# Performance work log

Hardware: AMD Instinct MI355X
Metric: run time of the kernel (lower is better)

Reference implementation:

```python
import jax, jax.numpy as jnp
import numpy as np

V, E, H, C, M, CLS = 32000, 300, 512, 256, 512, 1
B, T = 64, 128
NEG = -1e9


def setup_inputs() -> dict:
    key = jax.random.key(0)
    ks = jax.random.split(key, 16)
    u = lambda k, shape, r: jax.random.uniform(k, shape, jnp.float32, -r, r)
    klstm = 1.0 / np.sqrt(H)
    inp = {
        "s1": jax.random.randint(ks[0], (B, T), 0, V, dtype=jnp.int32),
        "s2": jax.random.randint(ks[1], (B, T), 0, V, dtype=jnp.int32),
        "s1_length": jax.random.randint(ks[2], (B,), 1, T + 1, dtype=jnp.int32),
        "s2_length": jax.random.randint(ks[3], (B,), 1, T + 1, dtype=jnp.int32),
        "s1_h0": jnp.zeros((2, B, H), jnp.float32),
        "s1_c0": jnp.zeros((2, B, H), jnp.float32),
        "s2_h0": jnp.zeros((2, B, H), jnp.float32),
        "s2_c0": jnp.zeros((2, B, H), jnp.float32),
        "emb": jax.random.normal(ks[4], (V, E), jnp.float32) * 0.1,
        "Wih_f": u(ks[5], (4 * H, E), klstm),
        "Whh_f": u(ks[6], (4 * H, H), klstm),
        "b_f": u(ks[7], (4 * H,), klstm),
        "Wih_b": u(ks[8], (4 * H, E), klstm),
        "Whh_b": u(ks[9], (4 * H, H), klstm),
        "b_b": u(ks[10], (4 * H,), klstm),
        "S1W": u(ks[11], (C, 2 * H), 0.1),
        "S2W": u(ks[12], (1, C), 0.1),
        "mlpW": u(ks[13], (M, 4 * H), 0.1),
        "mlpb": jnp.zeros((M,), jnp.float32),
        "outW": u(ks[14], (CLS, M), 0.1),
        "outb": jnp.zeros((CLS,), jnp.float32),
    }
    return inp


def lstm(x, h0, c0, Wih, Whh, b):
    # x: [B,T,E] -> outputs [B,T,H]; PyTorch gate order i,f,g,o
    xW = jnp.einsum("bte,ge->btg", x, Wih) + b  # [B,T,4H]

    def step(carry, xw):
        h, c = carry
        g = xw + h @ Whh.T
        i, f, gg, o = jnp.split(g, 4, axis=-1)
        c = jax.nn.sigmoid(f) * c + jax.nn.sigmoid(i) * jnp.tanh(gg)
        h = jax.nn.sigmoid(o) * jnp.tanh(c)
        return (h, c), h

    _, hs = jax.lax.scan(step, (h0, c0), jnp.swapaxes(xW, 0, 1))
    return jnp.swapaxes(hs, 0, 1)


def encode(tokens, lens, h0, c0, emb, Wih_f, Whh_f, b_f, Wih_b, Whh_b, b_b, S1W, S2W):
    x = emb[tokens]  # [B,T,E]
    t = jnp.arange(tokens.shape[1])
    # reverse-within-valid-length indices (pack/pad semantics for bwd direction)
    idx = jnp.where(t[None, :] < lens[:, None], lens[:, None] - 1 - t[None, :], t[None, :])
    out_f = lstm(x, h0[0], c0[0], Wih_f, Whh_f, b_f)
    x_rev = jnp.take_along_axis(x, idx[:, :, None], axis=1)
    out_b = lstm(x_rev, h0[1], c0[1], Wih_b, Whh_b, b_b)
    out_b = jnp.take_along_axis(out_b, idx[:, :, None], axis=1)
    Hout = jnp.concatenate([out_f, out_b], axis=-1)  # [B,T,2H]
    # attention pooling: S2(tanh(S1(H))), softmax over valid positions
    scores = jnp.einsum("btc,c->bt", jnp.tanh(jnp.einsum("btd,cd->btc", Hout, S1W)), S2W[0])
    scores = jnp.where(t[None, :] < lens[:, None], scores, NEG)
    attn = jax.nn.softmax(scores, axis=1)
    return jnp.einsum("bt,btd->bd", attn, Hout)  # [B,2H]


def reference(s1, s2, s1_length, s2_length, s1_h0, s1_c0, s2_h0, s2_c0, emb,
              Wih_f, Whh_f, b_f, Wih_b, Whh_b, b_b, S1W, S2W, mlpW, mlpb, outW, outb):
    r1 = encode(s1, s1_length, s1_h0, s1_c0, emb, Wih_f, Whh_f, b_f, Wih_b, Whh_b, b_b, S1W, S2W)
    r2 = encode(s2, s2_length, s2_h0, s2_c0, emb, Wih_f, Whh_f, b_f, Wih_b, Whh_b, b_b, S1W, S2W)
    merged = jnp.concatenate([r1 + r2, (r1 - r2) ** 2], axis=1)  # [B,4H]
    out_mlp = merged @ mlpW.T + mlpb  # no activation, per original
    return jax.nn.sigmoid(out_mlp @ outW.T + outb)  # [B,CLS]
```

## Files before the change

### kernel.cpp

```cpp
#include <hip/hip_runtime.h>
#include <hip/hip_bf16.h>

#define B_  64
#define T_  128
#define E_  300
#define EP  320
#define H_  512
#define G4  2048
#define R_  128
#define C_  256
#define M_  512
#define TS  (T_ + 1)
#define NB  128
#define SENT 0xFFFFFFFFFFFFFFFFULL

typedef short bf16x8 __attribute__((ext_vector_type(8)));
typedef float f32x4  __attribute__((ext_vector_type(4)));
#define MFMA(a, b, c) __builtin_amdgcn_mfma_f32_16x16x32_bf16((a), (b), (c), 0, 0, 0)

__device__ __forceinline__ float fsig(float x) { return 1.0f / (1.0f + __expf(-x)); }
__device__ __forceinline__ float ftanh(float x) {
    float a = fminf(fabsf(x), 15.0f);
    float e = __expf(2.0f * a);
    return copysignf((e - 1.0f) / (e + 1.0f), x);
}
__device__ __forceinline__ ushort f2bf(float f) {
    __hip_bfloat16 h = __float2bfloat16(f);
    return *reinterpret_cast<ushort*>(&h);
}
__device__ __forceinline__ float bf2f(ushort u) {
    __hip_bfloat16 h = *reinterpret_cast<__hip_bfloat16*>(&u);
    return __bfloat162float(h);
}

__global__ __launch_bounds__(256) void k_cvt_all(
    const float* __restrict__ emb,
    const float* __restrict__ Wih_f, const float* __restrict__ Wih_b,
    const float* __restrict__ Whh_f, const float* __restrict__ Whh_b,
    const float* __restrict__ S1W,
    const float* __restrict__ s1_h0, const float* __restrict__ s2_h0,
    ushort* __restrict__ embB,
    ushort* __restrict__ WihBf, ushort* __restrict__ WihBb,
    ushort* __restrict__ WhhBf, ushort* __restrict__ WhhBb,
    ushort* __restrict__ S1WB,
    ushort* __restrict__ hfB, ushort* __restrict__ hbB)
{
    const int b = blockIdx.x;
    if (b >= 5056) {
        const int r = b - 5056;
        const int rl = (r < B_) ? r : r - B_;
        const float* h0 = (r < B_) ? s1_h0 : s2_h0;
        for (int u = threadIdx.x; u < 128; u += 256) {
            const int which = u >> 6;
            const int c8 = (u & 63) * 8;
            const float* s = h0 + (long)which * B_ * H_ + (long)rl * H_ + c8;
            ushort* d = (which ? hbB : hfB) + (long)r * TS * H_ + c8;
            float4 f0 = *(const float4*)&s[0];
            float4 f1 = *(const float4*)&s[4];
            bf16x8 v;
            v[0] = (short)f2bf(f0.x); v[1] = (short)f2bf(f0.y);
            v[2] = (short)f2bf(f0.z); v[3] = (short)f2bf(f0.w);
            v[4] = (short)f2bf(f1.x); v[5] = (short)f2bf(f1.y);
            v[6] = (short)f2bf(f1.z); v[7] = (short)f2bf(f1.w);
            *(bf16x8*)d = v;
        }
        return;
    }
    const float* src; ushort* dst; int r0, sk, dk;
    if (b < 4000)      { src = emb;   dst = embB;  r0 = b * 8;          sk = E_;    dk = EP; }
    else if (b < 4256) { src = Wih_f; dst = WihBf; r0 = (b - 4000) * 8; sk = E_;    dk = EP; }
    else if (b < 4512) { src = Wih_b; dst = WihBb; r0 = (b - 4256) * 8; sk = E_;    dk = EP; }
    else if (b < 4768) { src = Whh_f; dst = WhhBf; r0 = (b - 4512) * 8; sk = H_;    dk = H_; }
    else if (b < 5024) { src = Whh_b; dst = WhhBb; r0 = (b - 4768) * 8; sk = H_;    dk = H_; }
    else               { src = S1W;   dst = S1WB;  r0 = (b - 5024) * 8; sk = 2*H_;  dk = 2*H_; }
    const int upr = dk >> 3;
    for (int u = threadIdx.x; u < 8 * upr; u += 256) {
        const int r  = r0 + u / upr;
        const int c8 = (u % upr) * 8;
        const float* s = &src[(long)r * sk + c8];
        bf16x8 v;
        if (c8 + 8 <= sk) {
            float4 f0 = *(const float4*)&s[0];
            float4 f1 = *(const float4*)&s[4];
            v[0] = (short)f2bf(f0.x); v[1] = (short)f2bf(f0.y);
            v[2] = (short)f2bf(f0.z); v[3] = (short)f2bf(f0.w);
            v[4] = (short)f2bf(f1.x); v[5] = (short)f2bf(f1.y);
            v[6] = (short)f2bf(f1.z); v[7] = (short)f2bf(f1.w);
        } else {
#pragma unroll
            for (int e = 0; e < 8; ++e)
                v[e] = (c8 + e < sk) ? (short)f2bf(s[e]) : (short)0;
        }
        *(bf16x8*)&dst[(long)r * dk + c8] = v;
    }
}

__global__ __launch_bounds__(256) void k_embed_mfma(
    const int* __restrict__ s1, const int* __restrict__ s2,
    const int* __restrict__ l1, const int* __restrict__ l2,
    const ushort* __restrict__ embB,
    const ushort* __restrict__ WihBf, const ushort* __restrict__ WihBb,
    const float* __restrict__ b_f, const float* __restrict__ b_b,
    ushort* __restrict__ xf, ushort* __restrict__ xb)
{
    const int dir = blockIdx.z;
    const int r   = blockIdx.y >> 1;
    const int t0  = (blockIdx.y & 1) * 64;
    const int N0  = blockIdx.x * 256;
    const int L   = (r < B_) ? l1[r] : l2[r - B_];
    if (L <= t0) return;

    const int tid = threadIdx.x;
    const int lane = tid & 63, w = tid >> 6;
    const int wm = w & 1, wn = w >> 1;
    const int l15 = lane & 15, q8 = (lane >> 4) * 8;

    __shared__ int toks[64];
    __shared__ __align__(16) ushort As[64][72];
    __shared__ __align__(16) ushort Bs[256][72];

    if (tid < 64) {
        int t  = t0 + tid;
        int tt = dir ? ((t < L) ? (L - 1 - t) : t) : t;
        toks[tid] = (r < B_) ? s1[r * T_ + tt] : s2[(r - B_) * T_ + tt];
    }
    __syncthreads();

    const ushort* Wih  = dir ? WihBb : WihBf;
    const float*  bias = dir ? b_b : b_f;

    f32x4 acc[2][8] = {};

    for (int k0 = 0; k0 < EP; k0 += 64) {
#pragma unroll
        for (int p = 0; p < 2; ++p) {
            int u = tid + p * 256;
            int row = u >> 3, seg = u & 7;
            *(uint4*)&As[row][seg * 8] =
                *(const uint4*)&embB[(long)toks[row] * EP + k0 + seg * 8];
        }
#pragma unroll
        for (int p = 0; p < 8; ++p) {
            int u = tid + p * 256;
            int row = u >> 3, seg = u & 7;
            *(uint4*)&Bs[row][seg * 8] =
                *(const uint4*)&Wih[(long)(N0 + row) * EP + k0 + seg * 8];
        }
        __syncthreads();
#pragma unroll
        for (int ks = 0; ks < 2; ++ks) {
            bf16x8 af[2], bfr[8];
#pragma unroll
            for (int mt = 0; mt < 2; ++mt)
                af[mt] = *(const bf16x8*)&As[wm * 32 + mt * 16 + l15][ks * 32 + q8];
#pragma unroll
            for (int nt = 0; nt < 8; ++nt)
                bfr[nt] = *(const bf16x8*)&Bs[wn * 128 + nt * 16 + l15][ks * 32 + q8];
#pragma unroll
            for (int mt = 0; mt < 2; ++mt)
#pragma unroll
                for (int nt = 0; nt < 8; ++nt)
                    acc[mt][nt] = MFMA(af[mt], bfr[nt], acc[mt][nt]);
        }
        __syncthreads();
    }

    ushort* xout = dir ? xb : xf;
#pragma unroll
    for (int mt = 0; mt < 2; ++mt) {
        int m = r * T_ + t0 + wm * 32 + mt * 16 + (lane >> 4) * 4;
#pragma unroll
        for (int nt = 0; nt < 8; ++nt) {
            int col = N0 + wn * 128 + nt * 16 + l15;
            float bv = bias[col];
#pragma unroll
            for (int rg = 0; rg < 4; ++rg) {
                uint v = f2bf(acc[mt][nt][rg] + bv);
                uint pv = (uint)__shfl_xor((int)v, 1);
                if (!(lane & 1))
                    *(uint*)&xout[(long)(m + rg) * G4 + col] = v | (pv << 16);
            }
        }
    }
}

__global__ __launch_bounds__(256) void k_recur(
    const ushort* __restrict__ xf, const ushort* __restrict__ xb,
    ushort* __restrict__ hfB, ushort* __restrict__ hbB,
    const ushort* __restrict__ WhhBf, const ushort* __restrict__ WhhBb,
    const float* __restrict__ s1_c0, const float* __restrict__ s2_c0)
{
    const int bx = blockIdx.x;
    const int s  = bx >> 6;
    const int rb = (bx >> 4) & 3;
    const int jb = bx & 15;
    const int r0 = rb * 32, j0 = jb * 32;

    const ushort* xW  = s ? xb : xf;
    const ushort* Whh = s ? WhhBb : WhhBf;
    ushort* hB = s ? hbB : hfB;

    const int tid = threadIdx.x;
    const int lane = tid & 63;
    const int g = tid >> 6;
    const int l15 = lane & 15, q8 = (lane >> 4) * 8;

    __shared__ __align__(16) ushort As[32][520];
    __shared__ float Gs[4][32][33];

    bf16x8 bfr[2][16];
#pragma unroll
    for (int nt = 0; nt < 2; ++nt) {
        const ushort* brow = &Whh[((long)g * H_ + j0 + nt * 16 + l15) * H_];
#pragma unroll
        for (int ks = 0; ks < 16; ++ks)
            bfr[nt][ks] = *(const bf16x8*)&brow[ks * 32 + q8];
    }

    const int rr = tid >> 3, jj = (tid & 7) * 4;
    const int rg_ = r0 + rr;
    const int rl  = (rg_ < B_) ? rg_ : rg_ - B_;
    const float* c0p = (rg_ < B_) ? s1_c0 : s2_c0;
    float cst[4];
#pragma unroll
    for (int cc = 0; cc < 4; ++cc)
        cst[cc] = c0p[(long)s * B_ * H_ + (long)rl * H_ + j0 + jj + cc];

    const int arow = tid >> 3, aseg = tid & 7;
    const int swz = ((aseg + arow) & 7) * 8;

    for (int t = 0; t < T_; ++t) {
        uint2 xw[4];
        const long xbase = ((long)rg_ * T_ + t) * G4 + j0 + jj;
#pragma unroll
        for (int gg = 0; gg < 4; ++gg)
            xw[gg] = *(const uint2*)&xW[xbase + gg * H_];

        const ushort* hrow = &hB[((long)(r0 + arow) * TS + t) * H_ + aseg * 8];
        unsigned long long hv[16];
        bool ok;
        do {
#pragma unroll
            for (int i = 0; i < 16; ++i) {
                const unsigned long long* p8 =
                    (const unsigned long long*)(hrow + (i >> 1) * 64 + (i & 1) * 4);
                hv[i] = __hip_atomic_load(p8, __ATOMIC_RELAXED,
                                          __HIP_MEMORY_SCOPE_AGENT);
            }
            ok = true;
#pragma unroll
            for (int i = 0; i < 16; ++i)
                ok = ok && (hv[i] != SENT);
        } while (!ok);

#pragma unroll
        for (int sl = 0; sl < 8; ++sl) {
            uint4 av;
            av.x = (uint)hv[2 * sl];       av.y = (uint)(hv[2 * sl] >> 32);
            av.z = (uint)hv[2 * sl + 1];   av.w = (uint)(hv[2 * sl + 1] >> 32);
            *(uint4*)&As[arow][sl * 64 + swz] = av;
        }
        __syncthreads();

        f32x4 acc[2][2] = {};
#pragma unroll
        for (int ks = 0; ks < 16; ++ks) {
            const int e  = ks * 32 + q8;
            const int sl = e >> 6;
            const int c  = (e >> 3) & 7;
            bf16x8 a0 = *(const bf16x8*)&As[l15][sl * 64 + (((c + l15) & 7) << 3)];
            bf16x8 a1 = *(const bf16x8*)&As[16 + l15][sl * 64 + (((c + l15) & 7) << 3)];
            acc[0][0] = MFMA(a0, bfr[0][ks], acc[0][0]);
            acc[0][1] = MFMA(a0, bfr[1][ks], acc[0][1]);
            acc[1][0] = MFMA(a1, bfr[0][ks], acc[1][0]);
            acc[1][1] = MFMA(a1, bfr[1][ks], acc[1][1]);
        }

#pragma unroll
        for (int mt = 0; mt < 2; ++mt)
#pragma unroll
            for (int nt = 0; nt < 2; ++nt)
#pragma unroll
                for (int rg2 = 0; rg2 < 4; ++rg2)
                    Gs[g][mt * 16 + (lane >> 4) * 4 + rg2][nt * 16 + l15] =
                        acc[mt][nt][rg2];
        __syncthreads();

        ushort hp[4];
#pragma unroll
        for (int cc = 0; cc < 4; ++cc) {
            uint xv0 = (cc < 2) ? xw[0].x : xw[0].y;
            uint xv1 = (cc < 2) ? xw[1].x : xw[1].y;
            uint xv2 = (cc < 2) ? xw[2].x : xw[2].y;
            uint xv3 = (cc < 2) ? xw[3].x : xw[3].y;
            int sh = (cc & 1) * 16;
            float gi = Gs[0][rr][jj + cc] + bf2f((ushort)(xv0 >> sh));
            float gf = Gs[1][rr][jj + cc] + bf2f((ushort)(xv1 >> sh));
            float gg = Gs[2][rr][jj + cc] + bf2f((ushort)(xv2 >> sh));
            float go = Gs[3][rr][jj + cc] + bf2f((ushort)(xv3 >> sh));
            cst[cc] = fsig(gf) * cst[cc] + fsig(gi) * ftanh(gg);
            hp[cc] = f2bf(fsig(go) * ftanh(cst[cc]));
        }
        unsigned long long pk = (unsigned long long)hp[0]
                              | ((unsigned long long)hp[1] << 16)
                              | ((unsigned long long)hp[2] << 32)
                              | ((unsigned long long)hp[3] << 48);
        __hip_atomic_store(
            (unsigned long long*)&hB[((long)rg_ * TS + t + 1) * H_ + j0 + jj],
            pk, __ATOMIC_RELAXED, __HIP_MEMORY_SCOPE_AGENT);
    }
}

__global__ __launch_bounds__(256) void k_attn_fused(
    const ushort* __restrict__ hfB, const ushort* __restrict__ hbB,
    const int* __restrict__ l1, const int* __restrict__ l2,
    const ushort* __restrict__ S1WB, const float* __restrict__ S2W,
    float* __restrict__ pooled)
{
    const int r = blockIdx.x;
    const int L = (r < B_) ? l1[r] : l2[r - B_];
    const int tid = threadIdx.x;
    const int lane = tid & 63, w = tid >> 6;
    const int wm = w & 1, wn = w >> 1;
    const int l15 = lane & 15, q8 = (lane >> 4) * 8;

    __shared__ __align__(16) ushort As[128][72];
    __shared__ __align__(16) ushort Bs[256][72];
    __shared__ float sc[T_];
    __shared__ float att[T_];

    if (tid < T_) sc[tid] = 0.0f;

    f32x4 acc[4][8] = {};

    for (int k0 = 0; k0 < 2 * H_; k0 += 64) {
#pragma unroll
        for (int p = 0; p < 4; ++p) {
            int u = tid + p * 256;
            int row = u >> 3, seg = u & 7;
            int k = k0 + seg * 8;
            long idx;
            const ushort* src;
            if (k0 < H_) {
                src = hfB; idx = ((long)r * TS + row + 1) * H_ + k;
            } else {
                int tt = (row < L) ? (L - 1 - row) : row;
                src = hbB; idx = ((long)r * TS + tt + 1) * H_ + (k - H_);
            }
            *(uint4*)&As[row][seg * 8] = *(const uint4*)&src[idx];
        }
#pragma unroll
        for (int p = 0; p < 8; ++p) {
            int u = tid + p * 256;
            int row = u >> 3, seg = u & 7;
            *(uint4*)&Bs[row][seg * 8] =
                *(const uint4*)&S1WB[(long)row * (2 * H_) + k0 + seg * 8];
        }
        __syncthreads();
#pragma unroll
        for (int ks = 0; ks < 2; ++ks) {
            bf16x8 af[4], bfr[8];
#pragma unroll
            for (int mt = 0; mt < 4; ++mt)
                af[mt] = *(const bf16x8*)&As[wm * 64 + mt * 16 + l15][ks * 32 + q8];
#pragma unroll
            for (int nt = 0; nt < 8; ++nt)
                bfr[nt] = *(const bf16x8*)&Bs[wn * 128 + nt * 16 + l15][ks * 32 + q8];
#pragma unroll
            for (int mt = 0; mt < 4; ++mt)
#pragma unroll
                for (int nt = 0; nt < 8; ++nt)
                    acc[mt][nt] = MFMA(af[mt], bfr[nt], acc[mt][nt]);
        }
        __syncthreads();
    }

    float s2r[8];
#pragma unroll
    for (int nt = 0; nt < 8; ++nt)
        s2r[nt] = S2W[wn * 128 + nt * 16 + l15];
#pragma unroll
    for (int mt = 0; mt < 4; ++mt)
#pragma unroll
        for (int rg = 0; rg < 4; ++rg) {
            float v = 0.0f;
#pragma unroll
            for (int nt = 0; nt < 8; ++nt)
                v += ftanh(acc[mt][nt][rg]) * s2r[nt];
            v += __shfl_xor(v, 1);
            v += __shfl_xor(v, 2);
            v += __shfl_xor(v, 4);
            v += __shfl_xor(v, 8);
            if (l15 == 0)
                atomicAdd(&sc[wm * 64 + mt * 16 + (lane >> 4) * 4 + rg], v);
        }
    __syncthreads();

    float mx = -1e30f;
    for (int tt = 0; tt < L; ++tt) mx = fmaxf(mx, sc[tt]);
    __syncthreads();
    if (tid < T_) att[tid] = (tid < L) ? __expf(sc[tid] - mx) : 0.0f;
    __syncthreads();
    float sum = 0.0f;
    for (int tt = 0; tt < L; ++tt) sum += att[tt];
    float inv = 1.0f / sum;

    for (int p = tid; p < 512; p += 256) {
        float a0 = 0.0f, a1 = 0.0f;
        if (p < 256) {
            int d = p * 2;
            for (int tt = 0; tt < L; ++tt) {
                uint hv = *(const uint*)&hfB[((long)r * TS + tt + 1) * H_ + d];
                a0 += att[tt] * bf2f((ushort)(hv & 0xffff));
                a1 += att[tt] * bf2f((ushort)(hv >> 16));
            }
            pooled[(long)r * (2 * H_) + d]     = a0 * inv;
            pooled[(long)r * (2 * H_) + d + 1] = a1 * inv;
        } else {
            int d = (p - 256) * 2;
            for (int tt = 0; tt < L; ++tt) {
                uint hv = *(const uint*)&hbB[((long)r * TS + (L - tt)) * H_ + d];
                a0 += att[tt] * bf2f((ushort)(hv & 0xffff));
                a1 += att[tt] * bf2f((ushort)(hv >> 16));
            }
            pooled[(long)r * (2 * H_) + H_ + d]     = a0 * inv;
            pooled[(long)r * (2 * H_) + H_ + d + 1] = a1 * inv;
        }
    }
}

__global__ __launch_bounds__(256) void k_mlp1(
    const float* __restrict__ pooled,
    const float* __restrict__ mlpW, const float* __restrict__ mlpb,
    float* __restrict__ om)
{
    const int mg = blockIdx.x;
    const int b  = blockIdx.y;
    const int tid = threadIdx.x;
    const int lane = tid & 63, w = tid >> 6;

    __shared__ __align__(16) float sm[2048];

#pragma unroll
    for (int it = 0; it < 8; ++it) {
        int d = tid + it * 256;
        float v;
        if (d < 1024) {
            v = pooled[(long)b * 1024 + d] + pooled[(long)(B_ + b) * 1024 + d];
        } else {
            int dd = d - 1024;
            float x = pooled[(long)b * 1024 + dd] - pooled[(long)(B_ + b) * 1024 + dd];
            v = x * x;
        }
        sm[d] = v;
    }
    __syncthreads();

    for (int i = 0; i < 16; ++i) {
        int mm = mg * 64 + w * 16 + i;
        const float* wrow = &mlpW[(long)mm * 2048];
        float ax = 0.f, ay = 0.f, az = 0.f, aw = 0.f;
#pragma unroll
        for (int it = 0; it < 8; ++it) {
            int k = it * 256 + lane * 4;
            float4 wv = *(const float4*)&wrow[k];
            float4 sv = *(const float4*)&sm[k];
            ax += wv.x * sv.x; ay += wv.y * sv.y;
            az += wv.z * sv.z; aw += wv.w * sv.w;
        }
        float ssum = (ax + ay) + (az + aw);
        for (int off = 32; off; off >>= 1) ssum += __shfl_down(ssum, off);
        if (lane == 0) om[(long)b * M_ + mm] = ssum + mlpb[mm];
    }
}

__global__ __launch_bounds__(256) void k_final(
    const float* __restrict__ om,
    const float* __restrict__ outW, const float* __restrict__ outb,
    float* __restrict__ out)
{
    const int b = blockIdx.x;
    const int tid = threadIdx.x;
    __shared__ float red[256];
    float p = om[(long)b * M_ + tid] * outW[tid]
            + om[(long)b * M_ + 256 + tid] * outW[256 + tid];
    red[tid] = p;
    __syncthreads();
    for (int off = 128; off > 0; off >>= 1) {
        if (tid < off) red[tid] += red[tid + off];
        __syncthreads();
    }
    if (tid == 0) out[b] = 1.0f / (1.0f + __expf(-(red[0] + outb[0])));
}

extern "C" void kernel_launch(void* const* d_in, const int* in_sizes, int n_in,
                              void* d_out, int out_size, void* d_ws, size_t ws_size,
                              hipStream_t stream)
{
    const int*   s1    = (const int*)d_in[0];
    const int*   s2    = (const int*)d_in[1];
    const int*   l1    = (const int*)d_in[2];
    const int*   l2    = (const int*)d_in[3];
    const float* s1_h0 = (const float*)d_in[4];
    const float* s1_c0 = (const float*)d_in[5];
    const float* s2_h0 = (const float*)d_in[6];
    const float* s2_c0 = (const float*)d_in[7];
    const float* emb   = (const float*)d_in[8];
    const float* Wih_f = (const float*)d_in[9];
    const float* Whh_f = (const float*)d_in[10];
    const float* b_f   = (const float*)d_in[11];
    const float* Wih_b = (const float*)d_in[12];
    const float* Whh_b = (const float*)d_in[13];
    const float* b_b   = (const float*)d_in[14];
    const float* S1W   = (const float*)d_in[15];
    const float* S2W   = (const float*)d_in[16];
    const float* mlpW  = (const float*)d_in[17];
    const float* mlpb  = (const float*)d_in[18];
    const float* outW  = (const float*)d_in[19];
    const float* outb  = (const float*)d_in[20];
    float* out = (float*)d_out;

    ushort* p16 = (ushort*)d_ws;
    ushort* embB  = p16;  p16 += (long)32000 * EP;
    ushort* WihBf = p16;  p16 += (long)G4 * EP;
    ushort* WihBb = p16;  p16 += (long)G4 * EP;
    ushort* WhhBf = p16;  p16 += (long)G4 * H_;
    ushort* WhhBb = p16;  p16 += (long)G4 * H_;
    ushort* S1WB  = p16;  p16 += (long)C_ * 2 * H_;
    ushort* xf    = p16;  p16 += (long)R_ * T_ * G4;
    ushort* xb    = p16;  p16 += (long)R_ * T_ * G4;
    ushort* hfB   = p16;  p16 += (long)R_ * TS * H_;
    ushort* hbB   = p16;  p16 += (long)R_ * TS * H_;
    float* pf = (float*)p16;
    float* pooled = pf;   pf += (long)R_ * 2 * H_;
    float* om     = pf;   pf += (long)B_ * M_;

    hipMemsetAsync(hfB, 0xFF, (size_t)2 * R_ * TS * H_ * sizeof(ushort), stream);

    k_cvt_all<<<5184, 256, 0, stream>>>(emb, Wih_f, Wih_b, Whh_f, Whh_b, S1W,
                                        s1_h0, s2_h0,
                                        embB, WihBf, WihBb, WhhBf, WhhBb, S1WB,
                                        hfB, hbB);

    k_embed_mfma<<<dim3(8, 256, 2), 256, 0, stream>>>(
        s1, s2, l1, l2, embB, WihBf, WihBb, b_f, b_b, xf, xb);

    k_recur<<<NB, 256, 0, stream>>>(xf, xb, hfB, hbB, WhhBf, WhhBb,
                                    s1_c0, s2_c0);

    k_attn_fused<<<R_, 256, 0, stream>>>(hfB, hbB, l1, l2, S1WB, S2W, pooled);

    k_mlp1<<<dim3(8, B_), 256, 0, stream>>>(pooled, mlpW, mlpb, om);
    k_final<<<B_, 256, 0, stream>>>(om, outW, outb, out);
}
```

Baseline: 791.6 us.

## Fuse input projection into recurrent kernel, computing next step's xW during recurrence

Drops the separate embedding-projection GEMM kernel and its large xf/xb intermediate buffers. Each recurrent block now keeps its slice of Wih in LDS, gathers the next timestep's embeddings, and computes the input projection for step t+1 with MFMA while waiting inside the serial recurrence. This removes the global round trip for the precomputed gates and one kernel launch. In exchange it adds per-step work and LDS traffic to the latency-critical recurrent loop, and it raises LDS use (about 100KB per block).

```diff
diff --git a/kernel.cpp b/kernel.cpp
--- a/kernel.cpp
+++ b/kernel.cpp
@@ -95,97 +95,12 @@
     }
 }
 
-__global__ __launch_bounds__(256) void k_embed_mfma(
+__global__ __launch_bounds__(256, 1) void k_recur(
     const int* __restrict__ s1, const int* __restrict__ s2,
     const int* __restrict__ l1, const int* __restrict__ l2,
     const ushort* __restrict__ embB,
     const ushort* __restrict__ WihBf, const ushort* __restrict__ WihBb,
     const float* __restrict__ b_f, const float* __restrict__ b_b,
-    ushort* __restrict__ xf, ushort* __restrict__ xb)
-{
-    const int dir = blockIdx.z;
-    const int r   = blockIdx.y >> 1;
-    const int t0  = (blockIdx.y & 1) * 64;
-    const int N0  = blockIdx.x * 256;
-    const int L   = (r < B_) ? l1[r] : l2[r - B_];
-    if (L <= t0) return;
-
-    const int tid = threadIdx.x;
-    const int lane = tid & 63, w = tid >> 6;
-    const int wm = w & 1, wn = w >> 1;
-    const int l15 = lane & 15, q8 = (lane >> 4) * 8;
-
-    __shared__ int toks[64];
-    __shared__ __align__(16) ushort As[64][72];
-    __shared__ __align__(16) ushort Bs[256][72];
-
-    if (tid < 64) {
-        int t  = t0 + tid;
-        int tt = dir ? ((t < L) ? (L - 1 - t) : t) : t;
-        toks[tid] = (r < B_) ? s1[r * T_ + tt] : s2[(r - B_) * T_ + tt];
-    }
-    __syncthreads();
-
-    const ushort* Wih  = dir ? WihBb : WihBf;
-    const float*  bias = dir ? b_b : b_f;
-
-    f32x4 acc[2][8] = {};
-
-    for (int k0 = 0; k0 < EP; k0 += 64) {
-#pragma unroll
-        for (int p = 0; p < 2; ++p) {
-            int u = tid + p * 256;
-            int row = u >> 3, seg = u & 7;
-            *(uint4*)&As[row][seg * 8] =
-                *(const uint4*)&embB[(long)toks[row] * EP + k0 + seg * 8];
-        }
-#pragma unroll
-        for (int p = 0; p < 8; ++p) {
-            int u = tid + p * 256;
-            int row = u >> 3, seg = u & 7;
-            *(uint4*)&Bs[row][seg * 8] =
-                *(const uint4*)&Wih[(long)(N0 + row) * EP + k0 + seg * 8];
-        }
-        __syncthreads();
-#pragma unroll
-        for (int ks = 0; ks < 2; ++ks) {
-            bf16x8 af[2], bfr[8];
-#pragma unroll
-            for (int mt = 0; mt < 2; ++mt)
-                af[mt] = *(const bf16x8*)&As[wm * 32 + mt * 16 + l15][ks * 32 + q8];
-#pragma unroll
-            for (int nt = 0; nt < 8; ++nt)
-                bfr[nt] = *(const bf16x8*)&Bs[wn * 128 + nt * 16 + l15][ks * 32 + q8];
-#pragma unroll
-            for (int mt = 0; mt < 2; ++mt)
-#pragma unroll
-                for (int nt = 0; nt < 8; ++nt)
-                    acc[mt][nt] = MFMA(af[mt], bfr[nt], acc[mt][nt]);
-        }
-        __syncthreads();
-    }
-
-    ushort* xout = dir ? xb : xf;
-#pragma unroll
-    for (int mt = 0; mt < 2; ++mt) {
-        int m = r * T_ + t0 + wm * 32 + mt * 16 + (lane >> 4) * 4;
-#pragma unroll
-        for (int nt = 0; nt < 8; ++nt) {
-            int col = N0 + wn * 128 + nt * 16 + l15;
-            float bv = bias[col];
-#pragma unroll
-            for (int rg = 0; rg < 4; ++rg) {
-                uint v = f2bf(acc[mt][nt][rg] + bv);
-                uint pv = (uint)__shfl_xor((int)v, 1);
-                if (!(lane & 1))
-                    *(uint*)&xout[(long)(m + rg) * G4 + col] = v | (pv << 16);
-            }
-        }
-    }
-}
-
-__global__ __launch_bounds__(256) void k_recur(
-    const ushort* __restrict__ xf, const ushort* __restrict__ xb,
     ushort* __restrict__ hfB, ushort* __restrict__ hbB,
     const ushort* __restrict__ WhhBf, const ushort* __restrict__ WhhBb,
     const float* __restrict__ s1_c0, const float* __restrict__ s2_c0)
@@ -196,8 +111,9 @@
     const int jb = bx & 15;
     const int r0 = rb * 32, j0 = jb * 32;
 
-    const ushort* xW  = s ? xb : xf;
-    const ushort* Whh = s ? WhhBb : WhhBf;
+    const ushort* Whh  = s ? WhhBb : WhhBf;
+    const ushort* WihB = s ? WihBb : WihBf;
+    const float*  bias = s ? b_b : b_f;
     ushort* hB = s ? hbB : hfB;
 
     const int tid = threadIdx.x;
@@ -207,6 +123,11 @@
 
     __shared__ __align__(16) ushort As[32][520];
     __shared__ float Gs[4][32][33];
+    __shared__ __align__(16) ushort WihL[128 * 320];
+    __shared__ __align__(16) ushort Aemb[32 * 320];
+    __shared__ __align__(16) ushort xWs[4][32][36];
+    __shared__ int toks[32];
+    __shared__ int Ls[32];
 
     bf16x8 bfr[2][16];
 #pragma unroll
@@ -229,12 +150,66 @@
     const int arow = tid >> 3, aseg = tid & 7;
     const int swz = ((aseg + arow) & 7) * 8;
 
+    const float biasv0 = bias[g * H_ + j0 + l15];
+    const float biasv1 = bias[g * H_ + j0 + 16 + l15];
+    const int cr0 = g * 32 + l15, cr1 = g * 32 + 16 + l15;
+
+    if (tid < 32) {
+        int rg = r0 + tid;
+        int L = (rg < B_) ? l1[rg] : l2[rg - B_];
+        Ls[tid] = L;
+        int tt = s ? ((L > 0) ? L - 1 : 0) : 0;
+        toks[tid] = (rg < B_) ? s1[rg * T_ + tt] : s2[(rg - B_) * T_ + tt];
+    }
+    for (int u = tid; u < 5120; u += 256) {
+        int cr = u / 40, un = u % 40;
+        int grow = (cr >> 5) * H_ + j0 + (cr & 31);
+        int pos = (un >> 3) * 64 + ((((un & 7) + cr) & 7) << 3);
+        *(bf16x8*)&WihL[cr * 320 + pos] =
+            *(const bf16x8*)&WihB[(long)grow * EP + un * 8];
+    }
+    __syncthreads();
+    for (int u = tid; u < 1280; u += 256) {
+        int row = u / 40, un = u % 40;
+        int pos = (un >> 3) * 64 + ((((un & 7) + row) & 7) << 3);
+        *(bf16x8*)&Aemb[row * 320 + pos] =
+            *(const bf16x8*)&embB[(long)toks[row] * EP + un * 8];
+    }
+    __syncthreads();
+    {
+        f32x4 ax[2][2] = {};
+#pragma unroll
+        for (int kk = 0; kk < 10; ++kk) {
+            int e = kk * 32 + q8;
+            int sb = (e >> 6) * 64;
+            int ch = (e >> 3) & 7;
+            bf16x8 a0 = *(const bf16x8*)&Aemb[l15 * 320 + sb + (((ch + l15) & 7) << 3)];
+            bf16x8 a1 = *(const bf16x8*)&Aemb[(16 + l15) * 320 + sb + (((ch + 16 + l15) & 7) << 3)];
+            bf16x8 b0 = *(const bf16x8*)&WihL[cr0 * 320 + sb + (((ch + cr0) & 7) << 3)];
+            bf16x8 b1 = *(const bf16x8*)&WihL[cr1 * 320 + sb + (((ch + cr1) & 7) << 3)];
+            ax[0][0] = MFMA(a0, b0, ax[0][0]);
+            ax[0][1] = MFMA(a0, b1, ax[0][1]);
+            ax[1][0] = MFMA(a1, b0, ax[1][0]);
+            ax[1][1] = MFMA(a1, b1, ax[1][1]);
+        }
+#pragma unroll
+        for (int mt = 0; mt < 2; ++mt)
+#pragma unroll
+            for (int rgx = 0; rgx < 4; ++rgx) {
+                int row = mt * 16 + (lane >> 4) * 4 + rgx;
+                xWs[g][row][l15]      = f2bf(ax[mt][0][rgx] + biasv0);
+                xWs[g][row][16 + l15] = f2bf(ax[mt][1][rgx] + biasv1);
+            }
+    }
+    __syncthreads();
+
     for (int t = 0; t < T_; ++t) {
-        uint2 xw[4];
-        const long xbase = ((long)rg_ * T_ + t) * G4 + j0 + jj;
-#pragma unroll
-        for (int gg = 0; gg < 4; ++gg)
-            xw[gg] = *(const uint2*)&xW[xbase + gg * H_];
+        if (t + 1 < T_ && tid < 32) {
+            int L = Ls[tid], tq = t + 1;
+            int tt = s ? ((tq < L) ? L - 1 - tq : tq) : tq;
+            int rg = r0 + tid;
+            toks[tid] = (rg < B_) ? s1[rg * T_ + tt] : s2[(rg - B_) * T_ + tt];
+        }
 
         const ushort* hrow = &hB[((long)(r0 + arow) * TS + t) * H_ + aseg * 8];
         unsigned long long hv[16];
@@ -261,6 +236,11 @@
             *(uint4*)&As[arow][sl * 64 + swz] = av;
         }
         __syncthreads();
+
+        uint2 xwr[4];
+#pragma unroll
+        for (int gg = 0; gg < 4; ++gg)
+            xwr[gg] = *(const uint2*)&xWs[gg][rr][jj];
 
         f32x4 acc[2][2] = {};
 #pragma unroll
@@ -276,6 +256,15 @@
             acc[1][1] = MFMA(a1, bfr[1][ks], acc[1][1]);
         }
 
+        if (t + 1 < T_) {
+            for (int u = tid; u < 1280; u += 256) {
+                int row = u / 40, un = u % 40;
+                int pos = (un >> 3) * 64 + ((((un & 7) + row) & 7) << 3);
+                *(bf16x8*)&Aemb[row * 320 + pos] =
+                    *(const bf16x8*)&embB[(long)toks[row] * EP + un * 8];
+            }
+        }
+
 #pragma unroll
         for (int mt = 0; mt < 2; ++mt)
 #pragma unroll
@@ -286,13 +275,39 @@
                         acc[mt][nt][rg2];
         __syncthreads();
 
+        if (t + 1 < T_) {
+            f32x4 ax[2][2] = {};
+#pragma unroll
+            for (int kk = 0; kk < 10; ++kk) {
+                int e = kk * 32 + q8;
+                int sb = (e >> 6) * 64;
+                int ch = (e >> 3) & 7;
+                bf16x8 a0 = *(const bf16x8*)&Aemb[l15 * 320 + sb + (((ch + l15) & 7) << 3)];
+                bf16x8 a1 = *(const bf16x8*)&Aemb[(16 + l15) * 320 + sb + (((ch + 16 + l15) & 7) << 3)];
+                bf16x8 b0 = *(const bf16x8*)&WihL[cr0 * 320 + sb + (((ch + cr0) & 7) << 3)];
+                bf16x8 b1 = *(const bf16x8*)&WihL[cr1 * 320 + sb + (((ch + cr1) & 7) << 3)];
+                ax[0][0] = MFMA(a0, b0, ax[0][0]);
+                ax[0][1] = MFMA(a0, b1, ax[0][1]);
+                ax[1][0] = MFMA(a1, b0, ax[1][0]);
+                ax[1][1] = MFMA(a1, b1, ax[1][1]);
+            }
+#pragma unroll
+            for (int mt = 0; mt < 2; ++mt)
+#pragma unroll
+                for (int rgx = 0; rgx < 4; ++rgx) {
+                    int row = mt * 16 + (lane >> 4) * 4 + rgx;
+                    xWs[g][row][l15]      = f2bf(ax[mt][0][rgx] + biasv0);
+                    xWs[g][row][16 + l15] = f2bf(ax[mt][1][rgx] + biasv1);
+                }
+        }
+
         ushort hp[4];
 #pragma unroll
         for (int cc = 0; cc < 4; ++cc) {
-            uint xv0 = (cc < 2) ? xw[0].x : xw[0].y;
-            uint xv1 = (cc < 2) ? xw[1].x : xw[1].y;
-            uint xv2 = (cc < 2) ? xw[2].x : xw[2].y;
-            uint xv3 = (cc < 2) ? xw[3].x : xw[3].y;
+            uint xv0 = (cc < 2) ? xwr[0].x : xwr[0].y;
+            uint xv1 = (cc < 2) ? xwr[1].x : xwr[1].y;
+            uint xv2 = (cc < 2) ? xwr[2].x : xwr[2].y;
+            uint xv3 = (cc < 2) ? xwr[3].x : xwr[3].y;
             int sh = (cc & 1) * 16;
             float gi = Gs[0][rr][jj + cc] + bf2f((ushort)(xv0 >> sh));
             float gf = Gs[1][rr][jj + cc] + bf2f((ushort)(xv1 >> sh));
@@ -527,8 +542,6 @@
     ushort* WhhBf = p16;  p16 += (long)G4 * H_;
     ushort* WhhBb = p16;  p16 += (long)G4 * H_;
     ushort* S1WB  = p16;  p16 += (long)C_ * 2 * H_;
-    ushort* xf    = p16;  p16 += (long)R_ * T_ * G4;
-    ushort* xb    = p16;  p16 += (long)R_ * T_ * G4;
     ushort* hfB   = p16;  p16 += (long)R_ * TS * H_;
     ushort* hbB   = p16;  p16 += (long)R_ * TS * H_;
     float* pf = (float*)p16;
@@ -542,10 +555,8 @@
                                         embB, WihBf, WihBb, WhhBf, WhhBb, S1WB,
                                         hfB, hbB);
 
-    k_embed_mfma<<<dim3(8, 256, 2), 256, 0, stream>>>(
-        s1, s2, l1, l2, embB, WihBf, WihBb, b_f, b_b, xf, xb);
-
-    k_recur<<<NB, 256, 0, stream>>>(xf, xb, hfB, hbB, WhhBf, WhhBb,
+    k_recur<<<NB, 256, 0, stream>>>(s1, s2, l1, l2, embB, WihBf, WihBb,
+                                    b_f, b_b, hfB, hbB, WhhBf, WhhBb,
                                     s1_c0, s2_c0);
 
     k_attn_fused<<<R_, 256, 0, stream>>>(hfB, hbB, l1, l2, S1WB, S2W, pooled);
```

New measurement: 1.002 ms. 26.6% more time.
